# Kernel optimization log

Hardware: AMD Instinct MI355X
Metric: run time of the kernel (lower is better)

## Reference

```python
import jax, jax.numpy as jnp
import numpy as np

# Dims: batch, queries, graph nodes, text len, hidden, heads, layers, ffn
B, NQ, NN, T, D, H, LAYERS, FF = 16, 32, 128, 352, 768, 8, 6, 3072
L = NQ + NN + T          # 512 total sequence length
HD = D // H              # 96 head dim
NEG = -1e9               # additive mask value (HF uses dtype min; -1e9 is equivalent post-softmax)
LN_EPS = 1e-12           # BERT LayerNorm eps


def _ln(x, g, b):
    m = x.mean(-1, keepdims=True)
    v = ((x - m) ** 2).mean(-1, keepdims=True)
    return (x - m) * jax.lax.rsqrt(v + LN_EPS) * g + b


def setup_inputs() -> dict:
    key = jax.random.key(0)
    ks = iter(jax.random.split(key, 32))

    def nrm(shape, s=0.02):
        return jax.random.normal(next(ks), shape, jnp.float32) * s

    return {
        "graph_node_features": jax.random.normal(next(ks), (B, NN, D), jnp.float32),
        "text_embeds": jax.random.normal(next(ks), (B, T, D), jnp.float32),
        "text_atts": jnp.ones((B, T), jnp.int32),
        "graph_mask": jnp.ones((B, NN), jnp.int32),
        "query_tokens": nrm((1, NQ, D), 1.0),   # nn.Parameter(torch.randn(...))
        "gproj_w": nrm((D, D)), "gproj_b": jnp.zeros((D,)),
        "pos_emb": nrm((L, D)), "tok_emb": nrm((D,)),  # token_type row 0
        "emb_ln_g": jnp.ones((D,)), "emb_ln_b": jnp.zeros((D,)),
        "qkv_w": nrm((LAYERS, D, 3 * D)), "qkv_b": jnp.zeros((LAYERS, 3 * D)),
        "ao_w": nrm((LAYERS, D, D)), "ao_b": jnp.zeros((LAYERS, D)),
        "ln1_g": jnp.ones((LAYERS, D)), "ln1_b": jnp.zeros((LAYERS, D)),
        "ff1_w": nrm((LAYERS, D, FF)), "ff1_b": jnp.zeros((LAYERS, FF)),
        "ff2_w": nrm((LAYERS, FF, D)), "ff2_b": jnp.zeros((LAYERS, D)),
        "ln2_g": jnp.ones((LAYERS, D)), "ln2_b": jnp.zeros((LAYERS, D)),
    }


def _itg_bias(text_atts, graph_mask):
    # Build the custom ITG prefix-LM mask: bidirectional over [queries|graph],
    # causal over text, and queries/graph blocked from attending to text.
    keep = jnp.concatenate(
        [jnp.ones((B, NQ), jnp.int32), graph_mask, text_atts], axis=1)  # [B, L]
    ts = NQ + NN
    idx = jnp.arange(L)
    is_text = idx >= ts
    pair = (keep[:, :, None] * keep[:, None, :]).astype(bool)          # padding mask
    causal_ok = jnp.where(is_text[:, None] & is_text[None, :],
                          idx[:, None] >= idx[None, :], True)           # tril in text block
    block_ok = ~((~is_text)[:, None] & is_text[None, :])                # prefix cannot see text
    mask = pair & causal_ok & block_ok                                  # [B, L, L]
    return jnp.where(mask, 0.0, NEG)[:, None, :, :]                     # [B, 1, L, L]


def reference(graph_node_features, text_embeds, text_atts, graph_mask,
              query_tokens, gproj_w, gproj_b, pos_emb, tok_emb,
              emb_ln_g, emb_ln_b, qkv_w, qkv_b, ao_w, ao_b,
              ln1_g, ln1_b, ff1_w, ff1_b, ff2_w, ff2_b, ln2_g, ln2_b):
    gfeat = graph_node_features @ gproj_w + gproj_b
    qtok = jnp.broadcast_to(query_tokens, (B, NQ, D))
    x = jnp.concatenate([qtok, gfeat, text_embeds], axis=1)             # [B, L, D]
    bias = _itg_bias(text_atts, graph_mask)

    # BERT embeddings (inputs_embeds path): + position + token_type(0), LN (dropout off)
    x = _ln(x + pos_emb[None] + tok_emb, emb_ln_g, emb_ln_b)

    scale = 1.0 / np.sqrt(HD)
    for i in range(LAYERS):
        qkv = x @ qkv_w[i] + qkv_b[i]
        q, k, v = jnp.split(qkv, 3, axis=-1)
        q = q.reshape(B, L, H, HD)
        k = k.reshape(B, L, H, HD)
        v = v.reshape(B, L, H, HD)
        s = jnp.einsum('bqhd,bkhd->bhqk', q, k) * scale + bias
        p = jax.nn.softmax(s, axis=-1)
        ctx = jnp.einsum('bhqk,bkhd->bqhd', p, v).reshape(B, L, D)
        x = _ln(x + ctx @ ao_w[i] + ao_b[i], ln1_g[i], ln1_b[i])
        h = jax.nn.gelu(x @ ff1_w[i] + ff1_b[i], approximate=False)
        x = _ln(x + h @ ff2_w[i] + ff2_b[i], ln2_g[i], ln2_b[i])

    return x[:, NQ + NN:, :]   # text_feats [B, T, D]
```

## Files before the change

### kernel.cpp

```cpp
#include <hip/hip_runtime.h>
#include <math.h>

typedef __bf16 bf16;
typedef __bf16 bf16x8 __attribute__((ext_vector_type(8)));
typedef float f32x4 __attribute__((ext_vector_type(4)));

#define NQ   32
#define NN_  128
#define TT   352
#define DD   768
#define NH   8
#define HDIM 96
#define LSEQ 512
#define TSPLIT 160
#define FFD  3072
#define NLAYER 6
#define NBATCH 16

#define GLOAD(srcp, dstp)                                                     \
    __builtin_amdgcn_global_load_lds(                                         \
        (const __attribute__((address_space(1))) void*)(srcp),                \
        (__attribute__((address_space(3))) void*)(dstp), 16, 0, 0)

template <int ACT>
__global__ __launch_bounds__(256) void gemm_bt(
    const bf16* __restrict__ A, const bf16* __restrict__ Bt,
    bf16* __restrict__ C, const float* __restrict__ bias,
    int K, int lda, int ldb, int ldc, float alpha, int Nstore, size_t zstride)
{
    __shared__ __attribute__((aligned(16))) bf16 As[3 * 4096];
    __shared__ __attribute__((aligned(16))) bf16 Bs[3 * 4096];

    const int z = blockIdx.z;
    A  += (size_t)z * K;
    Bt += (size_t)z * K;
    C  += (size_t)z * zstride;

    const int n0 = blockIdx.x * 128, m0 = blockIdx.y * 128;
    const int t = threadIdx.x;
    const int w = t >> 6, l = t & 63;
    const int wm = w >> 1, wn = w & 1;
    const int lr = l & 15, quad = l >> 4;

    f32x4 acc[4][4] = {};

    const int f0 = w * 1024 + l * 8;
    const int ra0 = f0 >> 5, ca0 = f0 & 31;
    const int ra1 = (f0 + 512) >> 5, ca1 = (f0 + 512) & 31;
    const bf16* a0 = A  + (size_t)(m0 + ra0) * lda + ca0;
    const bf16* a1 = A  + (size_t)(m0 + ra1) * lda + ca1;
    const bf16* b0 = Bt + (size_t)(n0 + ra0) * ldb + ca0;
    const bf16* b1 = Bt + (size_t)(n0 + ra1) * ldb + ca1;

    const int nt = K >> 5;

    {
        bf16* pA = &As[w * 1024];
        bf16* pB = &Bs[w * 1024];
        GLOAD(a0, pA);        GLOAD(a1, pA + 512);
        GLOAD(b0, pB);        GLOAD(b1, pB + 512);
        pA += 4096;  pB += 4096;
        GLOAD(a0 + 32, pA);   GLOAD(a1 + 32, pA + 512);
        GLOAD(b0 + 32, pB);   GLOAD(b1 + 32, pB + 512);
    }

    int cb = 0, wb = 2;
    for (int T = 0; T < nt; ++T) {
        if (T == nt - 1) {
            asm volatile("s_waitcnt vmcnt(0)" ::: "memory");
        } else {
            asm volatile("s_waitcnt vmcnt(4)" ::: "memory");
        }
        __builtin_amdgcn_s_barrier();
        __builtin_amdgcn_sched_barrier(0);

        if (T + 2 < nt) {
            const int k0 = (T + 2) << 5;
            bf16* pA = &As[wb * 4096 + w * 1024];
            bf16* pB = &Bs[wb * 4096 + w * 1024];
            GLOAD(a0 + k0, pA);   GLOAD(a1 + k0, pA + 512);
            GLOAD(b0 + k0, pB);   GLOAD(b1 + k0, pB + 512);
        }

        const int cur = cb << 12;
        bf16x8 af[4], bf_[4];
#pragma unroll
        for (int i = 0; i < 4; ++i)
            af[i] = *(const bf16x8*)&As[cur + (wm * 64 + i * 16 + lr) * 32 + quad * 8];
#pragma unroll
        for (int j = 0; j < 4; ++j)
            bf_[j] = *(const bf16x8*)&Bs[cur + (wn * 64 + j * 16 + lr) * 32 + quad * 8];
#pragma unroll
        for (int i = 0; i < 4; ++i)
#pragma unroll
            for (int j = 0; j < 4; ++j)
                acc[i][j] = __builtin_amdgcn_mfma_f32_16x16x32_bf16(af[i], bf_[j], acc[i][j], 0, 0, 0);

        cb = (cb == 2) ? 0 : cb + 1;
        wb = (wb == 2) ? 0 : wb + 1;
    }

    const bool dob = (z == 0);
#pragma unroll
    for (int i = 0; i < 4; ++i) {
        const int grow = m0 + wm * 64 + i * 16 + quad * 4;
#pragma unroll
        for (int j = 0; j < 4; ++j) {
            const int gcol = n0 + wn * 64 + j * 16 + lr;
            if (gcol >= Nstore) continue;
            float bv = (bias && dob) ? bias[gcol] : 0.0f;
#pragma unroll
            for (int r = 0; r < 4; ++r) {
                float v = acc[i][j][r] * alpha + bv;
                if (ACT == 1) v = 0.5f * v * (1.0f + erff(v * 0.70710678118654752f));
                C[(size_t)(grow + r) * ldc + gcol] = (bf16)v;
            }
        }
    }
}

template <int ACT>
__global__ __launch_bounds__(512) void gemm_bt8(
    const bf16* __restrict__ A, const bf16* __restrict__ Bt,
    bf16* __restrict__ C, const float* __restrict__ bias,
    int K, int lda, int ldb, int ldc, float alpha, int Nstore)
{
    __shared__ __attribute__((aligned(16))) bf16 As[3 * 8192];
    __shared__ __attribute__((aligned(16))) bf16 Bs[3 * 4096];

    const int n0 = blockIdx.x * 128, m0 = blockIdx.y * 256;
    const int t = threadIdx.x;
    const int w = t >> 6, l = t & 63;
    const int wm = w >> 1, wn = w & 1;
    const int lr = l & 15, quad = l >> 4;

    f32x4 acc[4][4] = {};

    const int f0 = w * 512 + l * 8;
    const int ra0 = f0 >> 5,          ca0 = f0 & 31;
    const int ra1 = ((f0 + 4096) >> 5), ca1 = f0 & 31;
    const bf16* a0 = A  + (size_t)(m0 + ra0) * lda + ca0;
    const bf16* a1 = A  + (size_t)(m0 + ra1) * lda + ca1;
    const bf16* b0 = Bt + (size_t)(n0 + ra0) * ldb + ca0;

    const int nt = K >> 5;

    {
        bf16* pA = &As[w * 512];
        bf16* pB = &Bs[w * 512];
        GLOAD(a0, pA);        GLOAD(a1, pA + 4096);   GLOAD(b0, pB);
        pA += 8192;  pB += 4096;
        GLOAD(a0 + 32, pA);   GLOAD(a1 + 32, pA + 4096);  GLOAD(b0 + 32, pB);
    }

    int cb = 0, wb = 2;
    for (int T = 0; T < nt; ++T) {
        if (T == nt - 1) {
            asm volatile("s_waitcnt vmcnt(0)" ::: "memory");
        } else {
            asm volatile("s_waitcnt vmcnt(3)" ::: "memory");
        }
        __builtin_amdgcn_s_barrier();
        __builtin_amdgcn_sched_barrier(0);

        if (T + 2 < nt) {
            const int k0 = (T + 2) << 5;
            bf16* pA = &As[wb * 8192 + w * 512];
            bf16* pB = &Bs[wb * 4096 + w * 512];
            GLOAD(a0 + k0, pA);  GLOAD(a1 + k0, pA + 4096);  GLOAD(b0 + k0, pB);
        }

        const int curA = cb * 8192, curB = cb * 4096;
        bf16x8 af[4], bf_[4];
#pragma unroll
        for (int i = 0; i < 4; ++i)
            af[i] = *(const bf16x8*)&As[curA + (wm * 64 + i * 16 + lr) * 32 + quad * 8];
#pragma unroll
        for (int j = 0; j < 4; ++j)
            bf_[j] = *(const bf16x8*)&Bs[curB + (wn * 64 + j * 16 + lr) * 32 + quad * 8];

        __builtin_amdgcn_s_setprio(1);
#pragma unroll
        for (int i = 0; i < 4; ++i)
#pragma unroll
            for (int j = 0; j < 4; ++j)
                acc[i][j] = __builtin_amdgcn_mfma_f32_16x16x32_bf16(af[i], bf_[j], acc[i][j], 0, 0, 0);
        __builtin_amdgcn_s_setprio(0);

        cb = (cb == 2) ? 0 : cb + 1;
        wb = (wb == 2) ? 0 : wb + 1;
    }

#pragma unroll
    for (int i = 0; i < 4; ++i) {
        const int grow = m0 + wm * 64 + i * 16 + quad * 4;
#pragma unroll
        for (int j = 0; j < 4; ++j) {
            const int gcol = n0 + wn * 64 + j * 16 + lr;
            if (gcol >= Nstore) continue;
            float bv = bias ? bias[gcol] : 0.0f;
#pragma unroll
            for (int r = 0; r < 4; ++r) {
                float v = acc[i][j][r] * alpha + bv;
                if (ACT == 1) v = 0.5f * v * (1.0f + erff(v * 0.70710678118654752f));
                C[(size_t)(grow + r) * ldc + gcol] = (bf16)v;
            }
        }
    }
}

__global__ __launch_bounds__(256) void flash_attn(
    const bf16* __restrict__ qkv, bf16* __restrict__ ctx,
    const int* __restrict__ tatts, const int* __restrict__ gmask)
{
    __shared__ __attribute__((aligned(16))) bf16 Qs[64 * 104];
    __shared__ __attribute__((aligned(16))) bf16 Ks[64 * 104];
    __shared__ __attribute__((aligned(16))) bf16 Vs[96 * 72];
    __shared__ __attribute__((aligned(16))) bf16 Ps[64 * 72];
    __shared__ int keep[512];

    const int qt = blockIdx.x;
    const int bh = blockIdx.y;
    const int b = bh >> 3, h = bh & 7;
    const int q0 = qt * 64;
    const int t = threadIdx.x;
    const int w = t >> 6, l = t & 63;
    const int lr = l & 15, quad = l >> 4;
    const float scale = 0.10206207261596577f;

    const bf16* qbase = qkv + (size_t)b * 512 * 2304 + h * 96;
    const bf16* kbase = qbase + 768;
    const bf16* vbase = qbase + 1536;

    for (int j = t; j < 512; j += 256)
        keep[j] = (j < NQ) ? 1 : (j < TSPLIT ? gmask[b * NN_ + j - NQ]
                                             : tatts[b * TT + j - TSPLIT]);

#pragma unroll
    for (int c = 0; c < 3; ++c) {
        const int idx = t * 8 + c * 2048;
        const int r = idx / 96, d = idx % 96;
        *(bf16x8*)&Qs[r * 104 + d] =
            *(const bf16x8*)&qbase[(size_t)(q0 + r) * 2304 + d];
    }
    __syncthreads();

    int ki[4];
    int ig[4];
#pragma unroll
    for (int r = 0; r < 4; ++r) {
        ig[r] = q0 + w * 16 + quad * 4 + r;
        ki[r] = keep[ig[r]];
    }

    float m_run[4] = {-1e30f, -1e30f, -1e30f, -1e30f};
    float l_run[4] = {0.f, 0.f, 0.f, 0.f};
    f32x4 oc[6] = {};

    const int JMAX = (qt < 3) ? 128 : q0;
    for (int j0 = 0; j0 <= JMAX; j0 += 64) {
        __syncthreads();
#pragma unroll
        for (int c = 0; c < 3; ++c) {
            const int idx = t * 8 + c * 2048;
            const int r = idx / 96, d = idx % 96;
            *(bf16x8*)&Ks[r * 104 + d] =
                *(const bf16x8*)&kbase[(size_t)(j0 + r) * 2304 + d];
            bf16x8 vv = *(const bf16x8*)&vbase[(size_t)(j0 + r) * 2304 + d];
#pragma unroll
            for (int jj = 0; jj < 8; ++jj)
                Vs[(d + jj) * 72 + r] = vv[jj];
        }
        __syncthreads();

        bf16x8 aq[3];
#pragma unroll
        for (int ds = 0; ds < 3; ++ds)
            aq[ds] = *(const bf16x8*)&Qs[(w * 16 + lr) * 104 + ds * 32 + quad * 8];
        f32x4 sc[4];
#pragma unroll
        for (int cb = 0; cb < 4; ++cb) {
            f32x4 a = {};
#pragma unroll
            for (int ds = 0; ds < 3; ++ds) {
                bf16x8 bk = *(const bf16x8*)&Ks[(cb * 16 + lr) * 104 + ds * 32 + quad * 8];
                a = __builtin_amdgcn_mfma_f32_16x16x32_bf16(aq[ds], bk, a, 0, 0, 0);
            }
            sc[cb] = a;
        }

        float tm[4] = {-1e30f, -1e30f, -1e30f, -1e30f};
#pragma unroll
        for (int cb = 0; cb < 4; ++cb) {
            const int jg = j0 + cb * 16 + lr;
            const int kj = keep[jg];
#pragma unroll
            for (int r = 0; r < 4; ++r) {
                const int i = ig[r];
                bool ok = ki[r] && kj;
                if (i < TSPLIT && jg >= TSPLIT) ok = false;
                if (i >= TSPLIT && jg >= TSPLIT && i < jg) ok = false;
                float s = sc[cb][r] * scale + (ok ? 0.f : -1e9f);
                sc[cb][r] = s;
                tm[r] = fmaxf(tm[r], s);
            }
        }
#pragma unroll
        for (int off = 1; off < 16; off <<= 1)
#pragma unroll
            for (int r = 0; r < 4; ++r)
                tm[r] = fmaxf(tm[r], __shfl_xor(tm[r], off));

        float alpha_[4], ts[4] = {0.f, 0.f, 0.f, 0.f};
#pragma unroll
        for (int r = 0; r < 4; ++r) {
            const float mn = fmaxf(m_run[r], tm[r]);
            alpha_[r] = __expf(m_run[r] - mn);
            m_run[r] = mn;
            l_run[r] *= alpha_[r];
        }
#pragma unroll
        for (int db = 0; db < 6; ++db)
#pragma unroll
            for (int r = 0; r < 4; ++r)
                oc[db][r] *= alpha_[r];

#pragma unroll
        for (int cb = 0; cb < 4; ++cb)
#pragma unroll
            for (int r = 0; r < 4; ++r) {
                const float p = __expf(sc[cb][r] - m_run[r]);
                ts[r] += p;
                Ps[(w * 16 + quad * 4 + r) * 72 + cb * 16 + lr] = (bf16)p;
            }
#pragma unroll
        for (int off = 1; off < 16; off <<= 1)
#pragma unroll
            for (int r = 0; r < 4; ++r)
                ts[r] += __shfl_xor(ts[r], off);
#pragma unroll
        for (int r = 0; r < 4; ++r) l_run[r] += ts[r];

        __syncthreads();

#pragma unroll
        for (int l0 = 0; l0 < 64; l0 += 32) {
            bf16x8 ap = *(const bf16x8*)&Ps[(w * 16 + lr) * 72 + l0 + quad * 8];
#pragma unroll
            for (int db = 0; db < 6; ++db) {
                bf16x8 bv = *(const bf16x8*)&Vs[(db * 16 + lr) * 72 + l0 + quad * 8];
                oc[db] = __builtin_amdgcn_mfma_f32_16x16x32_bf16(ap, bv, oc[db], 0, 0, 0);
            }
        }
    }

#pragma unroll
    for (int r = 0; r < 4; ++r) {
        const float inv = 1.f / l_run[r];
        bf16* orow = ctx + ((size_t)b * 512 + ig[r]) * 768 + h * 96;
#pragma unroll
        for (int db = 0; db < 6; ++db)
            orow[db * 16 + lr] = (bf16)(oc[db][r] * inv);
    }
}

__global__ void transpose_w(const float* __restrict__ in, bf16* __restrict__ out,
                            int R, int C)
{
    __shared__ bf16 tile[32][33];
    const int c0 = blockIdx.x * 32, r0 = blockIdx.y * 32;
    const int tx = threadIdx.x & 31, ty = threadIdx.x >> 5;
    for (int i = ty; i < 32; i += 8)
        tile[i][tx] = (bf16)in[(size_t)(r0 + i) * C + c0 + tx];
    __syncthreads();
    for (int i = ty; i < 32; i += 8)
        out[(size_t)(c0 + i) * R + r0 + tx] = tile[tx][i];
}

__global__ void cvt_bf16(const float* __restrict__ in, bf16* __restrict__ out, int n)
{
    const int idx = blockIdx.x * 256 + threadIdx.x;
    if (idx < n) out[idx] = (bf16)in[idx];
}

__device__ __forceinline__ void block_reduce_2(float& a, float& b)
{
#pragma unroll
    for (int off = 32; off; off >>= 1) {
        a += __shfl_xor(a, off);
        b += __shfl_xor(b, off);
    }
    __shared__ float sa[4], sb[4];
    const int w = threadIdx.x >> 6;
    if ((threadIdx.x & 63) == 0) { sa[w] = a; sb[w] = b; }
    __syncthreads();
    a = sa[0] + sa[1] + sa[2] + sa[3];
    b = sb[0] + sb[1] + sb[2] + sb[3];
}

__global__ void embed_ln(const float* __restrict__ qtok, const bf16* __restrict__ gfeat,
                         const float* __restrict__ text, const float* __restrict__ pos,
                         const float* __restrict__ tok, const float* __restrict__ g,
                         const float* __restrict__ bb, bf16* __restrict__ x)
{
    const int row = blockIdx.x;
    const int l = row & 511, b = row >> 9;
    const int t = threadIdx.x;

    float vals[3], s = 0.f, sq = 0.f;
#pragma unroll
    for (int c = 0; c < 3; ++c) {
        const int d = t + c * 256;
        float base;
        if (l < NQ)           base = qtok[(size_t)l * DD + d];
        else if (l < TSPLIT)  base = (float)gfeat[((size_t)b * NN_ + (l - NQ)) * DD + d];
        else                  base = text[((size_t)b * TT + (l - TSPLIT)) * DD + d];
        float v = base + pos[(size_t)l * DD + d] + tok[d];
        vals[c] = v; s += v; sq += v * v;
    }
    block_reduce_2(s, sq);
    const float mean = s * (1.f / 768.f);
    const float var = sq * (1.f / 768.f) - mean * mean;
    const float rs = rsqrtf(var + 1e-12f);
    bf16* o = x + (size_t)row * DD;
#pragma unroll
    for (int c = 0; c < 3; ++c) {
        const int d = t + c * 256;
        o[d] = (bf16)((vals[c] - mean) * rs * g[d] + bb[d]);
    }
}

__global__ void ln_rows3(const bf16* __restrict__ X, const bf16* __restrict__ Y,
                         const bf16* __restrict__ Z, bf16* __restrict__ Out,
                         const float* __restrict__ g, const float* __restrict__ bb)
{
    const int row = blockIdx.x;
    const int t = threadIdx.x;
    const bf16* xr = X + (size_t)row * DD;
    const bf16* yr = Y + (size_t)row * DD;
    const bf16* zr = Z + (size_t)row * DD;
    float vals[3], s = 0.f, sq = 0.f;
#pragma unroll
    for (int c = 0; c < 3; ++c) {
        const int d = t + c * 256;
        float v = (float)xr[d] + (float)yr[d] + (float)zr[d];
        vals[c] = v; s += v; sq += v * v;
    }
    block_reduce_2(s, sq);
    const float mean = s * (1.f / 768.f);
    const float var = sq * (1.f / 768.f) - mean * mean;
    const float rs = rsqrtf(var + 1e-12f);
    bf16* o = Out + (size_t)row * DD;
#pragma unroll
    for (int c = 0; c < 3; ++c) {
        const int d = t + c * 256;
        o[d] = (bf16)((vals[c] - mean) * rs * g[d] + bb[d]);
    }
}

__global__ void copy_out(const bf16* __restrict__ x, float* __restrict__ out)
{
    const size_t idx = (size_t)blockIdx.x * 256 + threadIdx.x;
    const int d = idx % DD;
    const size_t row = idx / DD;
    const int t = row % TT;
    const int b = row / TT;
    out[idx] = (float)x[((size_t)b * LSEQ + TSPLIT + t) * DD + d];
}

static void launch_gemm(const bf16* A, const bf16* Bt, bf16* C, const float* bias,
                        int M, int K, int lda, int ldb, int ldc,
                        float alpha, int Nstore, int act, int ksplit, size_t zstride,
                        hipStream_t stream)
{
    dim3 grid((Nstore + 127) / 128, M / 128, ksplit);
    if (act)
        gemm_bt<1><<<grid, 256, 0, stream>>>(A, Bt, C, bias, K / ksplit, lda, ldb, ldc, alpha, Nstore, zstride);
    else
        gemm_bt<0><<<grid, 256, 0, stream>>>(A, Bt, C, bias, K / ksplit, lda, ldb, ldc, alpha, Nstore, zstride);
}

static void launch_gemm8(const bf16* A, const bf16* Bt, bf16* C, const float* bias,
                         int M, int K, int lda, int ldb, int ldc,
                         float alpha, int Nstore, int act, hipStream_t stream)
{
    dim3 grid((Nstore + 127) / 128, M / 256, 1);
    if (act)
        gemm_bt8<1><<<grid, 512, 0, stream>>>(A, Bt, C, bias, K, lda, ldb, ldc, alpha, Nstore);
    else
        gemm_bt8<0><<<grid, 512, 0, stream>>>(A, Bt, C, bias, K, lda, ldb, ldc, alpha, Nstore);
}

extern "C" void kernel_launch(void* const* d_in, const int* in_sizes, int n_in,
                              void* d_out, int out_size, void* d_ws, size_t ws_size,
                              hipStream_t stream)
{
    const float* gnf     = (const float*)d_in[0];
    const float* text    = (const float*)d_in[1];
    const int*   tatts   = (const int*)d_in[2];
    const int*   gmask   = (const int*)d_in[3];
    const float* qtok    = (const float*)d_in[4];
    const float* gproj_w = (const float*)d_in[5];
    const float* gproj_b = (const float*)d_in[6];
    const float* pos     = (const float*)d_in[7];
    const float* tok     = (const float*)d_in[8];
    const float* eg      = (const float*)d_in[9];
    const float* eb      = (const float*)d_in[10];
    const float* qkv_w   = (const float*)d_in[11];
    const float* qkv_b   = (const float*)d_in[12];
    const float* ao_w    = (const float*)d_in[13];
    const float* ao_b    = (const float*)d_in[14];
    const float* ln1g    = (const float*)d_in[15];
    const float* ln1b    = (const float*)d_in[16];
    const float* ff1_w   = (const float*)d_in[17];
    const float* ff1_b   = (const float*)d_in[18];
    const float* ff2_w   = (const float*)d_in[19];
    const float* ff2_b   = (const float*)d_in[20];
    const float* ln2g    = (const float*)d_in[21];
    const float* ln2b    = (const float*)d_in[22];
    float* out = (float*)d_out;

    bf16* ws   = (bf16*)d_ws;
    bf16* wt1  = ws;
    bf16* wt2  = wt1 + 2359296;
    bf16* x    = wt2 + 2359296;
    bf16* ctx  = x   + 6291456;
    bf16* t1   = ctx + 6291456;
    bf16* u    = t1  + 6291456;
    bf16* qkvb = u;
    bf16* hbuf = u;
    bf16* t2   = u   + 25165824;
    bf16* gfeat = t1;
    bf16* gnfb  = u;
    const size_t ZST = (size_t)(t2 - t1);

    dim3 blk(256);

    cvt_bf16<<<6144, blk, 0, stream>>>(gnf, gnfb, 1572864);
    transpose_w<<<dim3(24, 24), blk, 0, stream>>>(gproj_w, wt1, 768, 768);
    launch_gemm(gnfb, wt1, gfeat, gproj_b, 2048, 768, 768, 768, 768,
                1.f, 768, 0, 1, 0, stream);
    embed_ln<<<8192, blk, 0, stream>>>(qtok, gfeat, text, pos, tok, eg, eb, x);

    for (int i = 0; i < NLAYER; ++i) {
        transpose_w<<<dim3(72, 24), blk, 0, stream>>>(
            qkv_w + (size_t)i * 768 * 2304, wt1, 768, 2304);
        launch_gemm8(x, wt1, qkvb, qkv_b + i * 2304,
                     8192, 768, 768, 768, 2304, 1.f, 2304, 0, stream);
        flash_attn<<<dim3(8, 128), blk, 0, stream>>>(qkvb, ctx, tatts, gmask);
        transpose_w<<<dim3(24, 24), blk, 0, stream>>>(
            ao_w + (size_t)i * 589824, wt1, 768, 768);
        launch_gemm(ctx, wt1, t1, ao_b + i * 768,
                    8192, 768, 768, 768, 768, 1.f, 768, 0, 2, ZST, stream);
        ln_rows3<<<8192, blk, 0, stream>>>(x, t1, t2, x, ln1g + i * 768, ln1b + i * 768);

        transpose_w<<<dim3(96, 24), blk, 0, stream>>>(
            ff1_w + (size_t)i * 2359296, wt1, 768, 3072);
        transpose_w<<<dim3(24, 96), blk, 0, stream>>>(
            ff2_w + (size_t)i * 2359296, wt2, 3072, 768);
        launch_gemm8(x, wt1, hbuf, ff1_b + i * 3072,
                     8192, 768, 768, 768, 3072, 1.f, 3072, 1, stream);
        launch_gemm(hbuf, wt2, t1, ff2_b + i * 768,
                    8192, 3072, 3072, 3072, 768, 1.f, 768, 0, 2, ZST, stream);
        ln_rows3<<<8192, blk, 0, stream>>>(x, t1, t2, x, ln2g + i * 768, ln2b + i * 768);
    }

    copy_out<<<16896, blk, 0, stream>>>(x, out);

    (void)in_sizes; (void)n_in; (void)out_size; (void)ws_size;
}
```

Before: 2.141 ms.

## Batch weight transposes, vectorize LayerNorm and output copy, add MFMA priority hints

Merges the four per-layer weight transposes into one launch, each writing to its own buffer. Rewrites ln_rows3 to handle one row per wavefront with vector loads and shuffle reductions, and vectorizes copy_out. Raises wave priority around the attention MFMA blocks and moves the QKV GEMM from the 256x128 gemm_bt8 kernel to the 128-tile gemm_bt kernel. Together these aim to cut launch count and memory-access overhead, at the cost of more workspace for the separate weight buffers and a QKV GEMM tile choice that may not suit the shape.

```diff
diff --git a/kernel.cpp b/kernel.cpp
--- a/kernel.cpp
+++ b/kernel.cpp
@@ -3,6 +3,7 @@
 
 typedef __bf16 bf16;
 typedef __bf16 bf16x8 __attribute__((ext_vector_type(8)));
+typedef __bf16 bf16x4 __attribute__((ext_vector_type(4)));
 typedef float f32x4 __attribute__((ext_vector_type(4)));
 
 #define NQ   32
@@ -137,10 +138,10 @@
     f32x4 acc[4][4] = {};
 
     const int f0 = w * 512 + l * 8;
-    const int ra0 = f0 >> 5,          ca0 = f0 & 31;
-    const int ra1 = ((f0 + 4096) >> 5), ca1 = f0 & 31;
+    const int ra0 = f0 >> 5,            ca0 = f0 & 31;
+    const int ra1 = ((f0 + 4096) >> 5);
     const bf16* a0 = A  + (size_t)(m0 + ra0) * lda + ca0;
-    const bf16* a1 = A  + (size_t)(m0 + ra1) * lda + ca1;
+    const bf16* a1 = A  + (size_t)(m0 + ra1) * lda + ca0;
     const bf16* b0 = Bt + (size_t)(n0 + ra0) * ldb + ca0;
 
     const int nt = K >> 5;
@@ -181,10 +182,12 @@
 
         __builtin_amdgcn_s_setprio(1);
 #pragma unroll
-        for (int i = 0; i < 4; ++i)
-#pragma unroll
-            for (int j = 0; j < 4; ++j)
-                acc[i][j] = __builtin_amdgcn_mfma_f32_16x16x32_bf16(af[i], bf_[j], acc[i][j], 0, 0, 0);
+        for (int i = 0; i < 4; ++i) {
+            acc[i][0] = __builtin_amdgcn_mfma_f32_16x16x32_bf16(af[i], bf_[0], acc[i][0], 0, 0, 0);
+            acc[i][1] = __builtin_amdgcn_mfma_f32_16x16x32_bf16(af[i], bf_[1], acc[i][1], 0, 0, 0);
+            acc[i][2] = __builtin_amdgcn_mfma_f32_16x16x32_bf16(af[i], bf_[2], acc[i][2], 0, 0, 0);
+            acc[i][3] = __builtin_amdgcn_mfma_f32_16x16x32_bf16(af[i], bf_[3], acc[i][3], 0, 0, 0);
+        }
         __builtin_amdgcn_s_setprio(0);
 
         cb = (cb == 2) ? 0 : cb + 1;
@@ -278,6 +281,7 @@
         for (int ds = 0; ds < 3; ++ds)
             aq[ds] = *(const bf16x8*)&Qs[(w * 16 + lr) * 104 + ds * 32 + quad * 8];
         f32x4 sc[4];
+        __builtin_amdgcn_s_setprio(1);
 #pragma unroll
         for (int cb = 0; cb < 4; ++cb) {
             f32x4 a = {};
@@ -288,6 +292,7 @@
             }
             sc[cb] = a;
         }
+        __builtin_amdgcn_s_setprio(0);
 
         float tm[4] = {-1e30f, -1e30f, -1e30f, -1e30f};
 #pragma unroll
@@ -343,6 +348,7 @@
 
         __syncthreads();
 
+        __builtin_amdgcn_s_setprio(1);
 #pragma unroll
         for (int l0 = 0; l0 < 64; l0 += 32) {
             bf16x8 ap = *(const bf16x8*)&Ps[(w * 16 + lr) * 72 + l0 + quad * 8];
@@ -352,6 +358,7 @@
                 oc[db] = __builtin_amdgcn_mfma_f32_16x16x32_bf16(ap, bv, oc[db], 0, 0, 0);
             }
         }
+        __builtin_amdgcn_s_setprio(0);
     }
 
 #pragma unroll
@@ -364,17 +371,44 @@
     }
 }
 
-__global__ void transpose_w(const float* __restrict__ in, bf16* __restrict__ out,
-                            int R, int C)
+__device__ __forceinline__ void tr_tile(const float* __restrict__ in,
+                                        bf16* __restrict__ out,
+                                        int R, int C, int bx, int by)
 {
     __shared__ bf16 tile[32][33];
-    const int c0 = blockIdx.x * 32, r0 = blockIdx.y * 32;
+    const int c0 = bx * 32, r0 = by * 32;
     const int tx = threadIdx.x & 31, ty = threadIdx.x >> 5;
     for (int i = ty; i < 32; i += 8)
         tile[i][tx] = (bf16)in[(size_t)(r0 + i) * C + c0 + tx];
     __syncthreads();
     for (int i = ty; i < 32; i += 8)
         out[(size_t)(c0 + i) * R + r0 + tx] = tile[tx][i];
+}
+
+__global__ void transpose_w(const float* __restrict__ in, bf16* __restrict__ out,
+                            int R, int C)
+{
+    tr_tile(in, out, R, C, blockIdx.x, blockIdx.y);
+}
+
+__global__ void transpose_all(const float* __restrict__ qw, const float* __restrict__ aw,
+                              const float* __restrict__ f1, const float* __restrict__ f2,
+                              bf16* __restrict__ oq, bf16* __restrict__ oa,
+                              bf16* __restrict__ o1, bf16* __restrict__ o2)
+{
+    int id = blockIdx.x;
+    if (id < 1728) {
+        tr_tile(qw, oq, 768, 2304, id % 72, id / 72);
+    } else if (id < 2304) {
+        id -= 1728;
+        tr_tile(aw, oa, 768, 768, id % 24, id / 24);
+    } else if (id < 4608) {
+        id -= 2304;
+        tr_tile(f1, o1, 768, 3072, id % 96, id / 96);
+    } else {
+        id -= 4608;
+        tr_tile(f2, o2, 3072, 768, id % 24, id / 24);
+    }
 }
 
 __global__ void cvt_bf16(const float* __restrict__ in, bf16* __restrict__ out, int n)
@@ -430,42 +464,77 @@
     }
 }
 
-__global__ void ln_rows3(const bf16* __restrict__ X, const bf16* __restrict__ Y,
-                         const bf16* __restrict__ Z, bf16* __restrict__ Out,
-                         const float* __restrict__ g, const float* __restrict__ bb)
-{
-    const int row = blockIdx.x;
-    const int t = threadIdx.x;
+__global__ __launch_bounds__(256) void ln_rows3(
+    const bf16* __restrict__ X, const bf16* __restrict__ Y,
+    const bf16* __restrict__ Z, bf16* __restrict__ Out,
+    const float* __restrict__ g, const float* __restrict__ bb)
+{
+    const int w = threadIdx.x >> 6, l = threadIdx.x & 63;
+    const int row = (blockIdx.x << 2) + w;
     const bf16* xr = X + (size_t)row * DD;
     const bf16* yr = Y + (size_t)row * DD;
     const bf16* zr = Z + (size_t)row * DD;
-    float vals[3], s = 0.f, sq = 0.f;
-#pragma unroll
-    for (int c = 0; c < 3; ++c) {
-        const int d = t + c * 256;
-        float v = (float)xr[d] + (float)yr[d] + (float)zr[d];
-        vals[c] = v; s += v; sq += v * v;
-    }
-    block_reduce_2(s, sq);
+
+    bf16x8 a0 = *(const bf16x8*)&xr[l * 8];
+    bf16x8 b0 = *(const bf16x8*)&yr[l * 8];
+    bf16x8 c0 = *(const bf16x8*)&zr[l * 8];
+    bf16x4 a1 = *(const bf16x4*)&xr[512 + l * 4];
+    bf16x4 b1 = *(const bf16x4*)&yr[512 + l * 4];
+    bf16x4 c1 = *(const bf16x4*)&zr[512 + l * 4];
+
+    float v[12], s = 0.f, sq = 0.f;
+#pragma unroll
+    for (int i = 0; i < 8; ++i) {
+        float t = (float)a0[i] + (float)b0[i] + (float)c0[i];
+        v[i] = t; s += t; sq += t * t;
+    }
+#pragma unroll
+    for (int i = 0; i < 4; ++i) {
+        float t = (float)a1[i] + (float)b1[i] + (float)c1[i];
+        v[8 + i] = t; s += t; sq += t * t;
+    }
+#pragma unroll
+    for (int off = 32; off; off >>= 1) {
+        s += __shfl_xor(s, off);
+        sq += __shfl_xor(sq, off);
+    }
     const float mean = s * (1.f / 768.f);
     const float var = sq * (1.f / 768.f) - mean * mean;
     const float rs = rsqrtf(var + 1e-12f);
-    bf16* o = Out + (size_t)row * DD;
-#pragma unroll
-    for (int c = 0; c < 3; ++c) {
-        const int d = t + c * 256;
-        o[d] = (bf16)((vals[c] - mean) * rs * g[d] + bb[d]);
-    }
+
+    f32x4 g0 = *(const f32x4*)&g[l * 8];
+    f32x4 g1 = *(const f32x4*)&g[l * 8 + 4];
+    f32x4 g2 = *(const f32x4*)&g[512 + l * 4];
+    f32x4 p0 = *(const f32x4*)&bb[l * 8];
+    f32x4 p1 = *(const f32x4*)&bb[l * 8 + 4];
+    f32x4 p2 = *(const f32x4*)&bb[512 + l * 4];
+
+    bf16x8 o0;
+    bf16x4 o1;
+#pragma unroll
+    for (int i = 0; i < 4; ++i) {
+        o0[i]     = (bf16)((v[i]     - mean) * rs * g0[i] + p0[i]);
+        o0[4 + i] = (bf16)((v[4 + i] - mean) * rs * g1[i] + p1[i]);
+        o1[i]     = (bf16)((v[8 + i] - mean) * rs * g2[i] + p2[i]);
+    }
+    bf16* orow = Out + (size_t)row * DD;
+    *(bf16x8*)&orow[l * 8] = o0;
+    *(bf16x4*)&orow[512 + l * 4] = o1;
 }
 
 __global__ void copy_out(const bf16* __restrict__ x, float* __restrict__ out)
 {
-    const size_t idx = (size_t)blockIdx.x * 256 + threadIdx.x;
-    const int d = idx % DD;
-    const size_t row = idx / DD;
-    const int t = row % TT;
-    const int b = row / TT;
-    out[idx] = (float)x[((size_t)b * LSEQ + TSPLIT + t) * DD + d];
+    const size_t i8 = ((size_t)blockIdx.x * 256 + threadIdx.x) * 8;
+    const int d = (int)(i8 % DD);
+    const size_t row = i8 / DD;
+    const int t = (int)(row % TT);
+    const int b = (int)(row / TT);
+    bf16x8 v = *(const bf16x8*)&x[((size_t)b * LSEQ + TSPLIT + t) * DD + d];
+    f32x4 o0, o1;
+#pragma unroll
+    for (int j = 0; j < 4; ++j) { o0[j] = (float)v[j]; o1[j] = (float)v[4 + j]; }
+    *(f32x4*)&out[i8] = o0;
+    *(f32x4*)&out[i8 + 4] = o1;
 }
 
 static void launch_gemm(const bf16* A, const bf16* Bt, bf16* C, const float* bias,
@@ -521,9 +590,11 @@
     float* out = (float*)d_out;
 
     bf16* ws   = (bf16*)d_ws;
-    bf16* wt1  = ws;
-    bf16* wt2  = wt1 + 2359296;
-    bf16* x    = wt2 + 2359296;
+    bf16* wq   = ws;
+    bf16* wa   = wq + 1769472;
+    bf16* w1   = wa + 589824;
+    bf16* w2   = w1 + 2359296;
+    bf16* x    = w2 + 2359296;
     bf16* ctx  = x   + 6291456;
     bf16* t1   = ctx + 6291456;
     bf16* u    = t1  + 6291456;
@@ -537,35 +608,32 @@
     dim3 blk(256);
 
     cvt_bf16<<<6144, blk, 0, stream>>>(gnf, gnfb, 1572864);
-    transpose_w<<<dim3(24, 24), blk, 0, stream>>>(gproj_w, wt1, 768, 768);
-    launch_gemm(gnfb, wt1, gfeat, gproj_b, 2048, 768, 768, 768, 768,
+    transpose_w<<<dim3(24, 24), blk, 0, stream>>>(gproj_w, w1, 768, 768);
+    launch_gemm(gnfb, w1, gfeat, gproj_b, 2048, 768, 768, 768, 768,
                 1.f, 768, 0, 1, 0, stream);
     embed_ln<<<8192, blk, 0, stream>>>(qtok, gfeat, text, pos, tok, eg, eb, x);
 
     for (int i = 0; i < NLAYER; ++i) {
-        transpose_w<<<dim3(72, 24), blk, 0, stream>>>(
-            qkv_w + (size_t)i * 768 * 2304, wt1, 768, 2304);
-        launch_gemm8(x, wt1, qkvb, qkv_b + i * 2304,
-                     8192, 768, 768, 768, 2304, 1.f, 2304, 0, stream);
+        transpose_all<<<6912, blk, 0, stream>>>(
+            qkv_w + (size_t)i * 768 * 2304, ao_w + (size_t)i * 589824,
+            ff1_w + (size_t)i * 2359296,    ff2_w + (size_t)i * 2359296,
+            wq, wa, w1, w2);
+
+        launch_gemm(x, wq, qkvb, qkv_b + i * 2304,
+                    8192, 768, 768, 768, 2304, 1.f, 2304, 0, 1, 0, stream);
         flash_attn<<<dim3(8, 128), blk, 0, stream>>>(qkvb, ctx, tatts, gmask);
-        transpose_w<<<dim3(24, 24), blk, 0, stream>>>(
-            ao_w + (size_t)i * 589824, wt1, 768, 768);
-        launch_gemm(ctx, wt1, t1, ao_b + i * 768,
+        launch_gemm(ctx, wa, t1, ao_b + i * 768,
                     8192, 768, 768, 768, 768, 1.f, 768, 0, 2, ZST, stream);
-        ln_rows3<<<8192, blk, 0, stream>>>(x, t1, t2, x, ln1g + i * 768, ln1b + i * 768);
-
-        transpose_w<<<dim3(96, 24), blk, 0, stream>>>(
-            ff1_w + (size_t)i * 2359296, wt1, 768, 3072);
-        transpose_w<<<dim3(24, 96), blk, 0, stream>>>(
-            ff2_w + (size_t)i * 2359296, wt2, 3072, 768);
-        launch_gemm8(x, wt1, hbuf, ff1_b + i * 3072,
+        ln_rows3<<<2048, blk, 0, stream>>>(x, t1, t2, x, ln1g + i * 768, ln1b + i * 768);
+
+        launch_gemm8(x, w1, hbuf, ff1_b + i * 3072,
                      8192, 768, 768, 768, 3072, 1.f, 3072, 1, stream);
-        launch_gemm(hbuf, wt2, t1, ff2_b + i * 768,
+        launch_gemm(hbuf, w2, t1, ff2_b + i * 768,
                     8192, 3072, 3072, 3072, 768, 1.f, 768, 0, 2, ZST, stream);
-        ln_rows3<<<8192, blk, 0, stream>>>(x, t1, t2, x, ln2g + i * 768, ln2b + i * 768);
-    }
-
-    copy_out<<<16896, blk, 0, stream>>>(x, out);
+        ln_rows3<<<2048, blk, 0, stream>>>(x, t1, t2, x, ln2g + i * 768, ln2b + i * 768);
+    }
+
+    copy_out<<<2112, blk, 0, stream>>>(x, out);
 
     (void)in_sizes; (void)n_in; (void)out_size; (void)ws_size;
 }
```

New measurement: 2.038 ms. 4.8% less time.
